# Optimization experiments

Hardware: AMD Instinct MI355X
Metric: run time of the kernel (lower is better)

Reference implementation:

```python
import jax, jax.numpy as jnp
import numpy as np

NUM_EXPERTS = 8
TOP_K = 2
BS, SL, HS, FFN = 4, 2048, 1024, 4096
CAPACITY_FACTOR = 1.0
# int(capacity_factor * top_k * tokens / num_experts)
EXPERT_CAPACITY = int(CAPACITY_FACTOR * TOP_K * BS * SL / NUM_EXPERTS)  # 4096


def setup_inputs() -> dict:
    key = jax.random.key(0)
    k0, k1, k2, k3, k4 = jax.random.split(key, 5)
    x = jax.random.normal(k0, (BS, SL, HS), jnp.float32)
    expert_weights = jax.random.uniform(k1, (BS * SL, TOP_K), jnp.float32)
    top_experts = jax.random.randint(k2, (BS * SL, TOP_K), 0, NUM_EXPERTS, dtype=jnp.int32)
    w1 = jax.random.normal(k3, (NUM_EXPERTS, HS, FFN), jnp.float32) * (HS ** -0.5)
    w2 = jax.random.normal(k4, (NUM_EXPERTS, FFN, HS), jnp.float32) * (FFN ** -0.5)
    bias = jnp.zeros((HS,), jnp.float32)
    return dict(x=x, expert_weights=expert_weights, w1=w1, w2=w2, bias=bias,
                top_experts=top_experts)


def reference(x, expert_weights, w1, w2, bias, top_experts):
    bs, sl, hs = x.shape
    E = w1.shape[0]
    k = top_experts.shape[-1]
    T = bs * sl
    cap = EXPERT_CAPACITY

    flat_x = x.reshape(T, hs)
    te = top_experts.reshape(-1)          # [T*k] expert assignment per (token, slot)
    ew = expert_weights.reshape(-1)       # [T*k]

    # indices_and_bins: stable radix sort by expert id + histogram + cumsum
    order = jnp.argsort(te)               # stable sort -> megablocks ops.sort indices
    bin_ids = te[order]
    tokens_per_expert = jnp.zeros((E,), jnp.int32).at[te].add(1)
    offsets = jnp.cumsum(tokens_per_expert) - tokens_per_expert  # exclusive cumsum
    pos = jnp.arange(T * k, dtype=jnp.int32) - offsets[bin_ids]  # rank within expert bin
    valid = pos < cap                     # tokens beyond expert_capacity are dropped
    token_idx = order // k                # source token for each sorted assignment

    # binned_gather -> [E, cap, hs]; dropped assignments go to a dump row
    e_idx = jnp.where(valid, bin_ids, E)
    p_idx = jnp.where(valid, pos, 0)
    gathered = jnp.zeros((E + 1, cap, hs), x.dtype).at[e_idx, p_idx].set(flat_x[token_idx])
    xg = gathered[:E]

    # grouped expert MLP: gelu(x @ w1) @ w2 per expert
    h = jax.nn.gelu(jnp.einsum('ech,ehf->ecf', xg, w1))
    out = jnp.einsum('ecf,efh->ech', h, w2)  # [E, cap, hs]

    # binned_scatter: gather expert outputs back, weight, sum top_k copies
    vals = out[bin_ids, p_idx] * (ew[order] * valid.astype(x.dtype))[:, None]
    y = jnp.zeros((T, hs), x.dtype).at[token_idx].add(vals)
    return y.reshape(bs, sl, hs) + bias
```

## Files before the change

### kernel.cpp

```cpp
#include <hip/hip_runtime.h>
#include <hip/hip_bf16.h>
#include <cstdint>

#define NE   8
#define TOPK 2
#define NT   8192
#define TK   16384
#define HS   1024
#define FFN  4096
#define CAP  2048

typedef float  f32x4  __attribute__((ext_vector_type(4)));
typedef __bf16 bf16x8 __attribute__((ext_vector_type(8)));
typedef __bf16 bf16x4 __attribute__((ext_vector_type(4)));

__device__ __forceinline__ void gload_lds16(const void* g, void* l) {
  __builtin_amdgcn_global_load_lds(
      (__attribute__((address_space(1))) void*)(void*)g,
      (__attribute__((address_space(3))) void*)l,
      16, 0, 0);
}

__global__ __launch_bounds__(1024)
void route_kernel(const int* __restrict__ te,
                  const float* __restrict__ ew,
                  int* __restrict__ asg_p,
                  float* __restrict__ asg_w,
                  int* __restrict__ slot_token) {
  const int e    = blockIdx.x;
  const int tid  = threadIdx.x;
  const int lane = tid & 63;
  const int w    = tid >> 6;
  __shared__ int wtot[16];
  int running = 0;
  for (int base = 0; base < TK; base += 1024) {
    const int i = base + tid;
    const int flag = (te[i] == e) ? 1 : 0;
    int val = flag;
    #pragma unroll
    for (int off = 1; off < 64; off <<= 1) {
      int n = __shfl_up(val, off);
      if (lane >= off) val += n;
    }
    if (lane == 63) wtot[w] = val;
    __syncthreads();
    int woff = 0, total = 0;
    #pragma unroll
    for (int j = 0; j < 16; j++) {
      const int t = wtot[j];
      if (j < w) woff += t;
      total += t;
    }
    if (flag) {
      const int p = running + woff + val - 1;
      asg_p[i] = p;
      const bool valid = (p < CAP);
      asg_w[i] = valid ? ew[i] : 0.0f;
      if (valid) slot_token[e * CAP + p] = i >> 1;
    }
    running += total;
    __syncthreads();
  }
}

__global__ void gather_kernel(const float* __restrict__ x,
                              const int* __restrict__ slot_token,
                              __bf16* __restrict__ Xg) {
  const int s   = blockIdx.x;
  const int tok = slot_token[s];
  const int idx = threadIdx.x * 4;
  bf16x4 o;
  if (tok >= 0) {
    const float4 v = *(const float4*)&x[(size_t)tok * HS + idx];
    o[0] = (__bf16)v.x; o[1] = (__bf16)v.y; o[2] = (__bf16)v.z; o[3] = (__bf16)v.w;
  } else {
    o[0] = (__bf16)0.f; o[1] = (__bf16)0.f; o[2] = (__bf16)0.f; o[3] = (__bf16)0.f;
  }
  *(bf16x4*)&Xg[(size_t)s * HS + idx] = o;
}

template<int R, int C>
__global__ void transpose_cast_kernel(const float* __restrict__ in,
                                      __bf16* __restrict__ out) {
  const int e = blockIdx.z;
  const float* in_e  = in  + (size_t)e * R * C;
  __bf16*      out_e = out + (size_t)e * R * C;
  const int c0 = blockIdx.x * 64;
  const int r0 = blockIdx.y * 64;
  __shared__ float tile[64][65];
  const int tid = threadIdx.x;
  const int lc = tid & 15, tr = tid >> 4;
  #pragma unroll
  for (int rr = 0; rr < 4; rr++) {
    const int row = rr * 16 + tr;
    const float4 v = *(const float4*)&in_e[(size_t)(r0 + row) * C + c0 + lc * 4];
    tile[row][lc * 4 + 0] = v.x; tile[row][lc * 4 + 1] = v.y;
    tile[row][lc * 4 + 2] = v.z; tile[row][lc * 4 + 3] = v.w;
  }
  __syncthreads();
  const int cb = tid & 7;
  #pragma unroll
  for (int p = 0; p < 2; p++) {
    const int orow = p * 32 + (tid >> 3);
    bf16x8 o;
    #pragma unroll
    for (int j = 0; j < 8; j++) o[j] = (__bf16)tile[cb * 8 + j][orow];
    *(bf16x8*)&out_e[(size_t)(c0 + orow) * R + r0 + cb * 8] = o;
  }
}

__device__ __forceinline__ float gelu_tanh(float v) {
  const float u = 0.7978845608028654f * (v + 0.044715f * v * v * v);
  const float t = 1.0f - 2.0f / (__expf(2.0f * u) + 1.0f);
  return 0.5f * v * (1.0f + t);
}

template<int DO_GELU, int MT_, int NT_>
__global__ __launch_bounds__(512, 2)
void gemm256_kernel(const __bf16* __restrict__ A,
                    const __bf16* __restrict__ B,
                    __bf16* __restrict__ C,
                    int N, int K) {
  const int bid = blockIdx.x;
  const int e   = bid & 7;
  const int g   = bid >> 3;
  const int s   = g >> 4;
  const int r   = g & 15;
  const int sm  = s % (MT_ / 4);
  const int sn  = s / (MT_ / 4);
  const int m0  = (sm * 4 + (r >> 2)) * 256;
  const int n0  = (sn * 4 + (r & 3)) * 256;

  const int tid  = threadIdx.x;
  const int lane = tid & 63;
  const int w    = tid >> 6;
  const int wm   = w >> 2;
  const int wn   = w & 3;

  __shared__ __align__(16) __bf16 ldsA[3][256 * 32];
  __shared__ __align__(16) __bf16 ldsB[3][256 * 32];

  const size_t Abase = ((size_t)e * CAP + m0) * (size_t)K;
  const size_t Bbase = (size_t)e * N * (size_t)K + (size_t)n0 * K;

  const int srow = w * 16 + (lane >> 2);
  const int scb  = (((lane & 3) ^ ((lane >> 3) & 3)) << 3);
  const __bf16* gA = A + Abase + (size_t)srow * K + scb;
  const __bf16* gB = B + Bbase + (size_t)srow * K + scb;
  const int ldst = w * 512;

  const int rA0  = wm * 128 + (lane & 15);
  const int rB0  = wn * 64  + (lane & 15);
  const int aoff = rA0 * 32 + ((((lane >> 4) ^ ((rA0 >> 1) & 3))) << 3);
  const int boff = rB0 * 32 + ((((lane >> 4) ^ ((rB0 >> 1) & 3))) << 3);

  f32x4 acc[8][4] = {};

  const int NKT = K >> 5;

#define STAGE_A(buf, kt) do {                                             \
    const __bf16* _g = gA + (size_t)(kt) * 32;                            \
    gload_lds16(_g,                    &ldsA[buf][ldst]);                 \
    gload_lds16(_g + (size_t)128 * K,  &ldsA[buf][4096 + ldst]);          \
  } while (0)
#define STAGE_B(buf, kt) do {                                             \
    const __bf16* _g = gB + (size_t)(kt) * 32;                            \
    gload_lds16(_g,                    &ldsB[buf][ldst]);                 \
    gload_lds16(_g + (size_t)128 * K,  &ldsB[buf][4096 + ldst]);          \
  } while (0)

  STAGE_A(0, 0); STAGE_B(0, 0);
  STAGE_A(1, 1); STAGE_B(1, 1);
  asm volatile("s_waitcnt vmcnt(4)" ::: "memory");
  __builtin_amdgcn_s_barrier();
  asm volatile("" ::: "memory");

  int cur = 0, stg = 2;
  for (int t = 0; t < NKT; ++t) {
    const bool do_stage = (t + 2 < NKT);
    bf16x8 aq[4], bq[4];

    #pragma unroll
    for (int i = 0; i < 4; ++i) bq[i] = *(const bf16x8*)&ldsB[cur][boff + i * 512];
    #pragma unroll
    for (int i = 0; i < 4; ++i) aq[i] = *(const bf16x8*)&ldsA[cur][aoff + i * 512];
    if (do_stage) STAGE_A(stg, t + 2);
    __builtin_amdgcn_s_barrier();
    asm volatile("s_waitcnt lgkmcnt(0)" ::: "memory");
    __builtin_amdgcn_s_setprio(1);
    #pragma unroll
    for (int mi = 0; mi < 4; ++mi)
      #pragma unroll
      for (int ni = 0; ni < 4; ++ni)
        acc[mi][ni] = __builtin_amdgcn_mfma_f32_16x16x32_bf16(aq[mi], bq[ni], acc[mi][ni], 0, 0, 0);
    __builtin_amdgcn_s_setprio(0);
    __builtin_amdgcn_s_barrier();
    asm volatile("" ::: "memory");

    #pragma unroll
    for (int i = 0; i < 4; ++i) aq[i] = *(const bf16x8*)&ldsA[cur][aoff + 2048 + i * 512];
    if (do_stage) STAGE_B(stg, t + 2);
    __builtin_amdgcn_s_barrier();
    asm volatile("s_waitcnt lgkmcnt(0)" ::: "memory");
    __builtin_amdgcn_s_setprio(1);
    #pragma unroll
    for (int mi = 0; mi < 4; ++mi)
      #pragma unroll
      for (int ni = 0; ni < 4; ++ni)
        acc[4 + mi][ni] = __builtin_amdgcn_mfma_f32_16x16x32_bf16(aq[mi], bq[ni], acc[4 + mi][ni], 0, 0, 0);
    __builtin_amdgcn_s_setprio(0);

    if (t + 1 < NKT) {
      if (do_stage) { asm volatile("s_waitcnt vmcnt(4)" ::: "memory"); }
      else          { asm volatile("s_waitcnt vmcnt(0)" ::: "memory"); }
      __builtin_amdgcn_s_barrier();
      asm volatile("" ::: "memory");
    }
    cur = (cur == 2) ? 0 : cur + 1;
    stg = (stg == 2) ? 0 : stg + 1;
  }
#undef STAGE_A
#undef STAGE_B

  const int crow = (lane >> 4) * 4;
  const int ccol = lane & 15;
  const size_t Crow0 = (size_t)e * CAP + m0 + wm * 128;
  #pragma unroll
  for (int mi = 0; mi < 8; ++mi) {
    #pragma unroll
    for (int ni = 0; ni < 4; ++ni) {
      const f32x4 d = acc[mi][ni];
      const int col = n0 + wn * 64 + ni * 16 + ccol;
      #pragma unroll
      for (int rr = 0; rr < 4; ++rr) {
        float v = d[rr];
        if (DO_GELU) v = gelu_tanh(v);
        C[(Crow0 + mi * 16 + crow + rr) * (size_t)N + col] = (__bf16)v;
      }
    }
  }
}

__global__ void combine_kernel(const __bf16* __restrict__ Out,
                               const int* __restrict__ te,
                               const int* __restrict__ asg_p,
                               const float* __restrict__ asg_w,
                               const float* __restrict__ bias,
                               float* __restrict__ y) {
  const int t   = blockIdx.x;
  const int idx = threadIdx.x * 4;
  f32x4 acc = *(const f32x4*)&bias[idx];
  #pragma unroll
  for (int j = 0; j < TOPK; j++) {
    const int i = t * TOPK + j;
    const float wgt = asg_w[i];
    if (wgt != 0.0f) {
      const int slot = te[i] * CAP + asg_p[i];
      const bf16x4 o = *(const bf16x4*)&Out[(size_t)slot * HS + idx];
      acc[0] += wgt * (float)o[0];
      acc[1] += wgt * (float)o[1];
      acc[2] += wgt * (float)o[2];
      acc[3] += wgt * (float)o[3];
    }
  }
  *(f32x4*)&y[(size_t)t * HS + idx] = acc;
}

static constexpr size_t OFF_SLOT = 0;
static constexpr size_t OFF_ASGP = 65536;
static constexpr size_t OFF_ASGW = 131072;
static constexpr size_t OFF_XG   = 196608;
static constexpr size_t OFF_W1T  = OFF_XG  + (size_t)TK * HS * 2;
static constexpr size_t OFF_W2T  = OFF_W1T + (size_t)NE * HS * FFN * 2;
static constexpr size_t OFF_H    = OFF_W2T + (size_t)NE * HS * FFN * 2;
static constexpr size_t OFF_OUT  = OFF_H   + (size_t)NE * CAP * FFN * 2;

extern "C" void kernel_launch(void* const* d_in, const int* in_sizes, int n_in,
                              void* d_out, int out_size, void* d_ws, size_t ws_size,
                              hipStream_t stream) {
  const float* x    = (const float*)d_in[0];
  const float* ew   = (const float*)d_in[1];
  const float* w1   = (const float*)d_in[2];
  const float* w2   = (const float*)d_in[3];
  const float* bias = (const float*)d_in[4];
  const int*   te   = (const int*)d_in[5];
  float* y = (float*)d_out;

  char* ws = (char*)d_ws;
  int*    slot_token = (int*)(ws + OFF_SLOT);
  int*    asg_p      = (int*)(ws + OFF_ASGP);
  float*  asg_w      = (float*)(ws + OFF_ASGW);
  __bf16* Xg         = (__bf16*)(ws + OFF_XG);
  __bf16* W1t        = (__bf16*)(ws + OFF_W1T);
  __bf16* W2t        = (__bf16*)(ws + OFF_W2T);
  __bf16* H          = (__bf16*)(ws + OFF_H);
  __bf16* Out        = (__bf16*)(ws + OFF_OUT);

  hipMemsetAsync(slot_token, 0xFF, (size_t)NE * CAP * sizeof(int), stream);

  route_kernel<<<NE, 1024, 0, stream>>>(te, ew, asg_p, asg_w, slot_token);

  transpose_cast_kernel<HS, FFN><<<dim3(FFN / 64, HS / 64, NE), 256, 0, stream>>>(w1, W1t);
  transpose_cast_kernel<FFN, HS><<<dim3(HS / 64, FFN / 64, NE), 256, 0, stream>>>(w2, W2t);

  gather_kernel<<<NE * CAP, 256, 0, stream>>>(x, slot_token, Xg);

  gemm256_kernel<1, 8, 16><<<NE * 8 * 16, 512, 0, stream>>>(Xg, W1t, H, FFN, HS);

  gemm256_kernel<0, 8, 4><<<NE * 8 * 4, 512, 0, stream>>>(H, W2t, Out, HS, FFN);

  combine_kernel<<<NT, 256, 0, stream>>>(Out, te, asg_p, asg_w, bias, y);
}
```

Measured before the change: 700.6 us.

## Restructure GEMM main loop into 4-stage LDS pipeline with register double-buffering

Reworks the grouped GEMM K-loop to use four LDS stages and ping-pong register fragments. The loop is unrolled by two so LDS reads for the next tile are issued before the MFMAs of the current tile, with one barrier per k-step instead of several. The goal is to hide LDS read latency and cut barrier stalls. In exchange it uses more shared memory, which may lower occupancy, and more VGPRs. The loop also assumes NKT is even, with a hand-written epilogue for the last two tiles.

```diff
diff --git a/kernel.cpp b/kernel.cpp
--- a/kernel.cpp
+++ b/kernel.cpp
@@ -137,8 +137,8 @@
   const int wm   = w >> 2;
   const int wn   = w & 3;
 
-  __shared__ __align__(16) __bf16 ldsA[3][256 * 32];
-  __shared__ __align__(16) __bf16 ldsB[3][256 * 32];
+  __shared__ __align__(16) __bf16 ldsA[4][256 * 32];
+  __shared__ __align__(16) __bf16 ldsB[4][256 * 32];
 
   const size_t Abase = ((size_t)e * CAP + m0) * (size_t)K;
   const size_t Bbase = (size_t)e * N * (size_t)K + (size_t)n0 * K;
@@ -158,69 +158,100 @@
 
   const int NKT = K >> 5;
 
-#define STAGE_A(buf, kt) do {                                             \
-    const __bf16* _g = gA + (size_t)(kt) * 32;                            \
-    gload_lds16(_g,                    &ldsA[buf][ldst]);                 \
-    gload_lds16(_g + (size_t)128 * K,  &ldsA[buf][4096 + ldst]);          \
-  } while (0)
-#define STAGE_B(buf, kt) do {                                             \
-    const __bf16* _g = gB + (size_t)(kt) * 32;                            \
-    gload_lds16(_g,                    &ldsB[buf][ldst]);                 \
-    gload_lds16(_g + (size_t)128 * K,  &ldsB[buf][4096 + ldst]);          \
-  } while (0)
-
-  STAGE_A(0, 0); STAGE_B(0, 0);
-  STAGE_A(1, 1); STAGE_B(1, 1);
+#define STAGE(co, kt) do {                                                \
+    const __bf16* _ga = gA + (size_t)(kt) * 32;                           \
+    const __bf16* _gb = gB + (size_t)(kt) * 32;                           \
+    gload_lds16(_ga,                   &ldsA[(co)][ldst]);                \
+    gload_lds16(_ga + (size_t)128 * K, &ldsA[(co)][4096 + ldst]);         \
+    gload_lds16(_gb,                   &ldsB[(co)][ldst]);                \
+    gload_lds16(_gb + (size_t)128 * K, &ldsB[(co)][4096 + ldst]);         \
+  } while (0)
+
+#define READ_BL(bq, al, co) do {                                          \
+    const __bf16* _pb = &ldsB[(co)][0];                                   \
+    const __bf16* _pa = &ldsA[(co)][0];                                   \
+    _Pragma("unroll") for (int _i = 0; _i < 4; ++_i)                      \
+      bq[_i] = *(const bf16x8*)&_pb[boff + _i * 512];                     \
+    _Pragma("unroll") for (int _i = 0; _i < 4; ++_i)                      \
+      al[_i] = *(const bf16x8*)&_pa[aoff + _i * 512];                     \
+  } while (0)
+
+#define READ_H(ah, co) do {                                               \
+    const __bf16* _pa = &ldsA[(co)][0];                                   \
+    _Pragma("unroll") for (int _i = 0; _i < 4; ++_i)                      \
+      ah[_i] = *(const bf16x8*)&_pa[aoff + 2048 + _i * 512];              \
+  } while (0)
+
+#define MFMA_L(al, bq) do {                                               \
+    _Pragma("unroll") for (int _m = 0; _m < 4; ++_m)                      \
+      _Pragma("unroll") for (int _n = 0; _n < 4; ++_n)                    \
+        acc[_m][_n] = __builtin_amdgcn_mfma_f32_16x16x32_bf16(            \
+            al[_m], bq[_n], acc[_m][_n], 0, 0, 0);                        \
+  } while (0)
+
+#define MFMA_H(ah, bq) do {                                               \
+    _Pragma("unroll") for (int _m = 0; _m < 4; ++_m)                      \
+      _Pragma("unroll") for (int _n = 0; _n < 4; ++_n)                    \
+        acc[4 + _m][_n] = __builtin_amdgcn_mfma_f32_16x16x32_bf16(        \
+            ah[_m], bq[_n], acc[4 + _m][_n], 0, 0, 0);                    \
+  } while (0)
+
+  bf16x8 bA[4], lA[4], bB[4], lB[4], hP[4];
+
+  STAGE(0, 0); STAGE(1, 1);
+
   asm volatile("s_waitcnt vmcnt(4)" ::: "memory");
   __builtin_amdgcn_s_barrier();
   asm volatile("" ::: "memory");
-
-  int cur = 0, stg = 2;
-  for (int t = 0; t < NKT; ++t) {
-    const bool do_stage = (t + 2 < NKT);
-    bf16x8 aq[4], bq[4];
-
-    #pragma unroll
-    for (int i = 0; i < 4; ++i) bq[i] = *(const bf16x8*)&ldsB[cur][boff + i * 512];
-    #pragma unroll
-    for (int i = 0; i < 4; ++i) aq[i] = *(const bf16x8*)&ldsA[cur][aoff + i * 512];
-    if (do_stage) STAGE_A(stg, t + 2);
-    __builtin_amdgcn_s_barrier();
-    asm volatile("s_waitcnt lgkmcnt(0)" ::: "memory");
-    __builtin_amdgcn_s_setprio(1);
-    #pragma unroll
-    for (int mi = 0; mi < 4; ++mi)
-      #pragma unroll
-      for (int ni = 0; ni < 4; ++ni)
-        acc[mi][ni] = __builtin_amdgcn_mfma_f32_16x16x32_bf16(aq[mi], bq[ni], acc[mi][ni], 0, 0, 0);
-    __builtin_amdgcn_s_setprio(0);
+  READ_BL(bA, lA, 0);
+  STAGE(2, 2);
+  __builtin_amdgcn_sched_barrier(0);
+
+  for (int t = 1; t <= NKT - 3; t += 2) {
+    asm volatile("s_waitcnt vmcnt(4)" ::: "memory");
     __builtin_amdgcn_s_barrier();
     asm volatile("" ::: "memory");
-
-    #pragma unroll
-    for (int i = 0; i < 4; ++i) aq[i] = *(const bf16x8*)&ldsA[cur][aoff + 2048 + i * 512];
-    if (do_stage) STAGE_B(stg, t + 2);
+    READ_BL(bB, lB, t & 3);
+    READ_H(hP, (t - 1) & 3);
+    STAGE((t + 2) & 3, t + 2);
+    __builtin_amdgcn_sched_barrier(0);
+    __builtin_amdgcn_s_setprio(1);
+    MFMA_L(lA, bA);
+    MFMA_H(hP, bA);
+    __builtin_amdgcn_s_setprio(0);
+
+    asm volatile("s_waitcnt vmcnt(4)" ::: "memory");
     __builtin_amdgcn_s_barrier();
-    asm volatile("s_waitcnt lgkmcnt(0)" ::: "memory");
+    asm volatile("" ::: "memory");
+    READ_BL(bA, lA, (t + 1) & 3);
+    READ_H(hP, t & 3);
+    if (t + 3 < NKT) STAGE((t + 3) & 3, t + 3);
+    __builtin_amdgcn_sched_barrier(0);
     __builtin_amdgcn_s_setprio(1);
-    #pragma unroll
-    for (int mi = 0; mi < 4; ++mi)
-      #pragma unroll
-      for (int ni = 0; ni < 4; ++ni)
-        acc[4 + mi][ni] = __builtin_amdgcn_mfma_f32_16x16x32_bf16(aq[mi], bq[ni], acc[4 + mi][ni], 0, 0, 0);
+    MFMA_L(lB, bB);
+    MFMA_H(hP, bB);
     __builtin_amdgcn_s_setprio(0);
-
-    if (t + 1 < NKT) {
-      if (do_stage) { asm volatile("s_waitcnt vmcnt(4)" ::: "memory"); }
-      else          { asm volatile("s_waitcnt vmcnt(0)" ::: "memory"); }
-      __builtin_amdgcn_s_barrier();
-      asm volatile("" ::: "memory");
-    }
-    cur = (cur == 2) ? 0 : cur + 1;
-    stg = (stg == 2) ? 0 : stg + 1;
-  }
-#undef STAGE_A
-#undef STAGE_B
+  }
+
+  asm volatile("s_waitcnt vmcnt(0)" ::: "memory");
+  __builtin_amdgcn_s_barrier();
+  asm volatile("" ::: "memory");
+  READ_BL(bB, lB, (NKT - 1) & 3);
+  READ_H(hP, (NKT - 2) & 3);
+  __builtin_amdgcn_sched_barrier(0);
+  __builtin_amdgcn_s_setprio(1);
+  MFMA_L(lA, bA);
+  MFMA_H(hP, bA);
+  READ_H(hP, (NKT - 1) & 3);
+  MFMA_L(lB, bB);
+  MFMA_H(hP, bB);
+  __builtin_amdgcn_s_setprio(0);
+
+#undef STAGE
+#undef READ_BL
+#undef READ_H
+#undef MFMA_L
+#undef MFMA_H
 
   const int crow = (lane >> 4) * 4;
   const int ccol = lane & 15;
```

After: 678.7 us. -3.1%, faster.
